# Kernel tuning notes

Measured on AMD Instinct MI355X. Metric: run time of the kernel, lower is better.

Reference implementation:

```python
import jax, jax.numpy as jnp
import numpy as np

D = 2048        # d_model
H = 16          # n_heads
HKV = 4         # n_kv_heads
DH = 128        # d_head = D // H
FF = int(D * 8 / 3)  # 5461, SwiGLU hidden
EPS = 1e-6
ROPE_BASE = 10000.0
B, L = 2, 2048


def rmsnorm(x, w):
    rms = jnp.sqrt(jnp.mean(x * x, axis=-1, keepdims=True) + EPS)
    return x / rms * w


def rope_cos_sin(seq_len):
    inv_freq = 1.0 / (ROPE_BASE ** (jnp.arange(0, DH, 2, dtype=jnp.float32) / DH))
    t = jnp.arange(seq_len, dtype=jnp.float32)
    freqs = t[:, None] * inv_freq[None, :]              # (L, DH/2)
    emb = jnp.concatenate([freqs, freqs], axis=-1)      # (L, DH)
    return jnp.cos(emb), jnp.sin(emb)


def rotate_half(x):
    x1, x2 = jnp.split(x, 2, axis=-1)
    return jnp.concatenate([-x2, x1], axis=-1)


def setup_inputs() -> dict:
    key = jax.random.key(0)
    ks = jax.random.split(key, 10)
    s = 0.02
    return {
        "x": jax.random.normal(ks[0], (B, L, D), dtype=jnp.float32),
        "w_norm1": jnp.ones((D,), dtype=jnp.float32),
        "wq": jax.random.normal(ks[1], (D, H * DH), dtype=jnp.float32) * s,
        "wk": jax.random.normal(ks[2], (D, HKV * DH), dtype=jnp.float32) * s,
        "wv": jax.random.normal(ks[3], (D, HKV * DH), dtype=jnp.float32) * s,
        "wo": jax.random.normal(ks[4], (H * DH, D), dtype=jnp.float32) * s,
        "w_norm2": jnp.ones((D,), dtype=jnp.float32),
        "w_gate": jax.random.normal(ks[5], (D, FF), dtype=jnp.float32) * s,
        "w_up": jax.random.normal(ks[6], (D, FF), dtype=jnp.float32) * s,
        "w_down": jax.random.normal(ks[7], (FF, D), dtype=jnp.float32) * s,
    }


def reference(x, w_norm1, wq, wk, wv, wo, w_norm2, w_gate, w_up, w_down):
    b, l, d = x.shape
    n_rep = H // HKV
    residual = x
    h = rmsnorm(x, w_norm1)
    q = (h @ wq).reshape(b, l, H, DH).transpose(0, 2, 1, 3)    # (B,H,L,DH)
    k = (h @ wk).reshape(b, l, HKV, DH).transpose(0, 2, 1, 3)  # (B,HKV,L,DH)
    v = (h @ wv).reshape(b, l, HKV, DH).transpose(0, 2, 1, 3)
    cos, sin = rope_cos_sin(l)                                 # (L,DH), broadcasts
    q = q * cos + rotate_half(q) * sin
    k = k * cos + rotate_half(k) * sin
    # GQA: repeat KV heads to match Q heads
    k = jnp.repeat(k, n_rep, axis=1)
    v = jnp.repeat(v, n_rep, axis=1)
    scale = 1.0 / np.sqrt(DH)
    attn = jnp.einsum('bhld,bhmd->bhlm', q, k) * scale         # (B,H,L,L)
    causal = jnp.triu(jnp.ones((l, l), dtype=bool), 1)
    attn = jnp.where(causal, -1e9, attn)
    attn = jax.nn.softmax(attn, axis=-1)
    out = jnp.einsum('bhlm,bhmd->bhld', attn, v)
    out = out.transpose(0, 2, 1, 3).reshape(b, l, d)
    x = residual + out @ wo
    residual = x
    h = rmsnorm(x, w_norm2)
    ffn = (jax.nn.silu(h @ w_gate) * (h @ w_up)) @ w_down
    return residual + ffn
```

## Files before the change

kernel.cpp:

```cpp
#include <hip/hip_runtime.h>
#include <stdint.h>

#define BATCH 2
#define SEQ   2048
#define DM    2048
#define NH    16
#define NKV   4
#define DHD   128
#define FFR   5461
#define FFP   5504
#define NTOK  (BATCH*SEQ)
#define QKVW  3072

typedef float f32x4 __attribute__((ext_vector_type(4)));
typedef short bf8v __attribute__((ext_vector_type(8)));
typedef unsigned short us8 __attribute__((ext_vector_type(8)));

__device__ __forceinline__ unsigned short f2bf(float f) {
  unsigned u = __float_as_uint(f);
  u += 0x7fff + ((u >> 16) & 1);
  return (unsigned short)(u >> 16);
}
__device__ __forceinline__ float bf2f(unsigned short b) {
  return __uint_as_float(((unsigned)b) << 16);
}

__device__ __forceinline__ void gload16(const void* g, void* l) {
  __builtin_amdgcn_global_load_lds(
      (const __attribute__((address_space(1))) unsigned int*)(uintptr_t)g,
      (__attribute__((address_space(3))) unsigned int*)(uintptr_t)l,
      16, 0, 0);
}

__global__ __launch_bounds__(256) void k_transpose(const float* __restrict__ S,
    unsigned short* __restrict__ T, int K, int N, int Kpad)
{
  __shared__ float tile[32][33];
  const int n0 = blockIdx.x << 5, k0 = blockIdx.y << 5;
  const int c = threadIdx.x & 31, r0 = threadIdx.x >> 5;
#pragma unroll
  for (int i = 0; i < 4; ++i) {
    int r = r0 + (i << 3);
    float v = 0.f;
    if ((k0 + r) < K && (n0 + c) < N) v = S[(long)(k0 + r) * N + n0 + c];
    tile[r][c] = v;
  }
  __syncthreads();
#pragma unroll
  for (int i = 0; i < 4; ++i) {
    int rr = r0 + (i << 3);
    T[(long)(n0 + rr) * Kpad + k0 + c] = f2bf(tile[c][rr]);
  }
}

__global__ __launch_bounds__(256) void k_transpose_fu(const float* __restrict__ S,
    unsigned short* __restrict__ T, int K, int N, int Kpad, int m01)
{
  __shared__ float tile[32][33];
  const int n0 = blockIdx.x << 5, k0 = blockIdx.y << 5;
  const int c = threadIdx.x & 31, r0 = threadIdx.x >> 5;
#pragma unroll
  for (int i = 0; i < 4; ++i) {
    int r = r0 + (i << 3);
    float v = 0.f;
    if ((k0 + r) < K && (n0 + c) < N) v = S[(long)(k0 + r) * N + n0 + c];
    tile[r][c] = v;
  }
  __syncthreads();
#pragma unroll
  for (int i = 0; i < 4; ++i) {
    int rr = r0 + (i << 3);
    int n = n0 + rr;
    long rp = (long)(n >> 6)*128 + ((n & 63) >> 4)*32 + m01*16 + (n & 15);
    T[rp * Kpad + k0 + c] = f2bf(tile[c][rr]);
  }
}

__global__ __launch_bounds__(256) void k_transpose_v(const unsigned short* __restrict__ KV,
    unsigned short* __restrict__ VT)
{
  __shared__ unsigned short tile[32][36];
  const int kv0 = blockIdx.x << 5, d0 = blockIdx.y << 5;
  const int bz = blockIdx.z;
  const int b = bz >> 2, hkv = bz & 3;
  const int flat = threadIdx.x * 4;
  const int r = flat >> 5, c = flat & 31;
  ushort4 v = *(const ushort4*)(KV + ((long)(b*SEQ + kv0 + r))*QKVW + 2560 + hkv*128 + d0 + c);
  tile[r][c] = v.x; tile[r][c+1] = v.y; tile[r][c+2] = v.z; tile[r][c+3] = v.w;
  __syncthreads();
  ushort4 o;
  o.x = tile[c][r]; o.y = tile[c+1][r]; o.z = tile[c+2][r]; o.w = tile[c+3][r];
  *(ushort4*)(VT + ((long)(bz*128 + d0 + r))*SEQ + kv0 + c) = o;
}

__global__ __launch_bounds__(256) void k_rmsnorm(const float* __restrict__ X,
    const float* __restrict__ W, unsigned short* __restrict__ H)
{
  __shared__ float red[4];
  const long row = blockIdx.x;
  const float* xr = X + row * DM;
  const int tid = threadIdx.x;
  float4 a0 = ((const float4*)xr)[2*tid];
  float4 a1 = ((const float4*)xr)[2*tid+1];
  float ss = a0.x*a0.x + a0.y*a0.y + a0.z*a0.z + a0.w*a0.w
           + a1.x*a1.x + a1.y*a1.y + a1.z*a1.z + a1.w*a1.w;
#pragma unroll
  for (int m = 32; m >= 1; m >>= 1) ss += __shfl_xor(ss, m, 64);
  if ((tid & 63) == 0) red[tid >> 6] = ss;
  __syncthreads();
  float sc = rsqrtf((red[0]+red[1]+red[2]+red[3]) * (1.0f/DM) + 1e-6f);
  float4 w0 = ((const float4*)W)[2*tid];
  float4 w1 = ((const float4*)W)[2*tid+1];
  us8 o;
  o[0]=f2bf(a0.x*sc*w0.x); o[1]=f2bf(a0.y*sc*w0.y); o[2]=f2bf(a0.z*sc*w0.z); o[3]=f2bf(a0.w*sc*w0.w);
  o[4]=f2bf(a1.x*sc*w1.x); o[5]=f2bf(a1.y*sc*w1.y); o[6]=f2bf(a1.z*sc*w1.z); o[7]=f2bf(a1.w*sc*w1.w);
  *(us8*)(H + row*DM + tid*8) = o;
}

__global__ void k_rope_table(float* __restrict__ C, float* __restrict__ S)
{
  int i = blockIdx.x * 256 + threadIdx.x;
  int pos = i >> 6, d = i & 63;
  double inv = exp(-(double)d * (9.210340371976184 / 64.0));
  double ang = (double)pos * inv;
  C[i] = (float)cos(ang);
  S[i] = (float)sin(ang);
}

__global__ __launch_bounds__(256) void k_rope_apply(unsigned short* __restrict__ Q,
    const float* __restrict__ C, const float* __restrict__ S, int nh, int stride, int head0)
{
  long i = (long)blockIdx.x * 256 + threadIdx.x;
  int d = (int)(i & 63);
  long t = i >> 6;
  int hh = (int)(t % nh);
  long bl = t / nh;
  int pos = (int)(bl & (SEQ-1));
  long base = bl * stride + head0 + hh*DHD;
  float c = C[pos*64 + d], s = S[pos*64 + d];
  float x1 = bf2f(Q[base + d]);
  float x2 = bf2f(Q[base + 64 + d]);
  Q[base + d]      = f2bf(x1*c - x2*s);
  Q[base + 64 + d] = f2bf(x2*c + x1*s);
}

template<int EPI>
__global__ __launch_bounds__(256) void k_gemm(const unsigned short* __restrict__ A,
    const unsigned short* __restrict__ BT, void* Cout, const float* __restrict__ Res,
    int K, int ldc)
{
  __shared__ __align__(16) unsigned short As[2][128*64];
  __shared__ __align__(16) unsigned short Bs[2][128*64];
  const int tid = threadIdx.x;
  const int l = tid & 63, w = tid >> 6;
  const int wr = w >> 1, wc = w & 1;
  const int nM = gridDim.x, nN = gridDim.y;
  const int nwg = nM * nN;
  const int bid = blockIdx.y * gridDim.x + blockIdx.x;
  const int q8 = nwg >> 3, r8 = nwg & 7, xcd = bid & 7, off8 = bid >> 3;
  const int wg = (xcd < r8 ? xcd*(q8+1) : r8*(q8+1) + (xcd - r8)*q8) + off8;
  const int colTiles = nM * 4;
  const int fullCols = nN >> 2, rem = nN & 3;
  int sc, inCol, wN;
  if (wg < fullCols * colTiles) { sc = wg / colTiles; inCol = wg % colTiles; wN = 4; }
  else { sc = fullCols; inCol = wg - fullCols * colTiles; wN = rem; }
  const int perSuper = 2 * wN;
  const int sm = inCol / perSuper, t8 = inCol % perSuper;
  const long m0 = (long)(sm*2 + t8 / wN) * 128;
  const long n0 = (long)(sc*4 + t8 % wN) * 128;
  const char* Ab = (const char*)(A + m0 * (long)K);
  const char* Bb = (const char*)(BT + n0 * (long)K);
  f32x4 acc[4][4] = {};
  const long ldab = (long)K * 2;
  const int nk = K >> 6;
  const int srow = w*32 + (l >> 3);
  const int scol = ((l & 7) ^ (srow & 7)) * 16;
  auto STAGE = [&](int buf, int kt) {
    const long kb = (long)kt * 128;
#pragma unroll
    for (int i = 0; i < 4; ++i) {
      gload16(Ab + (long)(srow + i*8)*ldab + kb + scol, &As[buf][(w*32 + i*8)*64]);
      gload16(Bb + (long)(srow + i*8)*ldab + kb + scol, &Bs[buf][(w*32 + i*8)*64]);
    }
  };
  STAGE(0, 0);
  __syncthreads();
  int cur = 0;
  for (int kt = 0; kt < nk; ++kt) {
    if (kt + 1 < nk) STAGE(cur ^ 1, kt + 1);
#pragma unroll
    for (int kk = 0; kk < 2; ++kk) {
      bf8v af[4], bfv[4];
#pragma unroll
      for (int m = 0; m < 4; ++m) {
        int r = wr*64 + m*16 + (l & 15);
        int offb = (kk*64 + (l >> 4)*16) ^ ((r & 7) << 4);
        af[m] = *(const bf8v*)((const char*)&As[cur][0] + r*128 + offb);
      }
#pragma unroll
      for (int n = 0; n < 4; ++n) {
        int cI = wc*64 + n*16 + (l & 15);
        int offb = (kk*64 + (l >> 4)*16) ^ ((cI & 7) << 4);
        bfv[n] = *(const bf8v*)((const char*)&Bs[cur][0] + cI*128 + offb);
      }
#pragma unroll
      for (int m = 0; m < 4; ++m)
#pragma unroll
        for (int n = 0; n < 4; ++n)
          acc[m][n] = __builtin_amdgcn_mfma_f32_16x16x32_bf16(af[m], bfv[n], acc[m][n], 0, 0, 0);
    }
    __syncthreads();
    cur ^= 1;
  }
  if (EPI == 3) {
#pragma unroll
    for (int m = 0; m < 4; ++m)
#pragma unroll
      for (int n = 0; n < 4; n += 2)
#pragma unroll
        for (int r = 0; r < 4; ++r) {
          long row = m0 + wr*64 + m*16 + (l >> 4)*4 + r;
          long col = (n0 >> 1) + (wc*2 + (n >> 1))*16 + (l & 15);
          float g = acc[m][n][r], u = acc[m][n+1][r];
          float sv = g / (1.f + __expf(-g));
          ((unsigned short*)Cout)[row * (long)ldc + col] = f2bf(sv * u);
        }
    return;
  }
#pragma unroll
  for (int m = 0; m < 4; ++m)
#pragma unroll
    for (int n = 0; n < 4; ++n)
#pragma unroll
      for (int r = 0; r < 4; ++r) {
        long row = m0 + wr*64 + m*16 + (l >> 4)*4 + r;
        long col = n0 + wc*64 + n*16 + (l & 15);
        long idx = row * (long)ldc + col;
        if (EPI == 0) ((unsigned short*)Cout)[idx] = f2bf(acc[m][n][r]);
        else          ((float*)Cout)[idx] = Res[idx] + acc[m][n][r];
      }
}

__global__ __launch_bounds__(512) void k_attn(const unsigned short* __restrict__ QKV,
    const unsigned short* __restrict__ VbT, unsigned short* __restrict__ O)
{
  __shared__ __align__(16) unsigned short Ks[2][64*128];
  __shared__ __align__(16) unsigned short Vs[2][128*64];
  __shared__ __align__(16) unsigned short Pl[8][16][64];
  const int tid = threadIdx.x, l = tid & 63, w = tid >> 6;
  const int b = blockIdx.z, h = blockIdx.y;
  const int hkv = h >> 2;
  const float scale = 0.08838834764831845f;
  const unsigned short* Kbase = QKV + (long)b*SEQ*QKVW + 2048 + hkv*128;
  const unsigned short* Vtb = VbT + ((long)(b*NKV + hkv))*128*SEQ;

  for (int half = 0; half < 2; ++half) {
    const int qt = half ? (15 - (int)blockIdx.x) : (int)blockIdx.x;
    const int q0 = qt << 7;
    bf8v qa[4];
    {
      const unsigned short* qp = QKV + ((long)(b*SEQ + q0 + w*16 + (l & 15)))*QKVW + h*DHD + (l >> 4)*8;
#pragma unroll
      for (int kk = 0; kk < 4; ++kk) qa[kk] = *(const bf8v*)(qp + kk*32);
    }
    float m_[4], s_[4];
    f32x4 o_[8] = {};
#pragma unroll
    for (int r = 0; r < 4; ++r) { m_[r] = -1e30f; s_[r] = 0.f; }
    const int T = 2*qt + 2;
    const int qmaxw = q0 + w*16 + 15;

    auto STAGE = [&](int buf, int t) {
      const int kv0 = t << 6;
#pragma unroll
      for (int i = 0; i < 2; ++i) {
        int r = w*8 + i*4 + (l >> 4);
        int blk = (l & 15) ^ (r & 7);
        gload16(Kbase + ((long)(kv0 + r))*QKVW + blk*8, &Ks[buf][(w*8 + i*4)*128]);
      }
#pragma unroll
      for (int i = 0; i < 2; ++i) {
        int r = w*16 + i*8 + (l >> 3);
        int blk = (l & 7) ^ (r & 7);
        gload16(Vtb + (long)r*SEQ + kv0 + blk*8, &Vs[buf][(w*16 + i*8)*64]);
      }
    };
    STAGE(0, 0);
    __syncthreads();
    int cur = 0;
    for (int t = 0; t < T; ++t) {
      const int kv0 = t << 6;
      if (t + 1 < T) STAGE(cur ^ 1, t + 1);
      if (kv0 <= qmaxw) {
        f32x4 sc4[4] = {};
        __builtin_amdgcn_s_setprio(1);
#pragma unroll
        for (int n = 0; n < 4; ++n) {
          int row = n*16 + (l & 15);
          const char* kr = (const char*)&Ks[cur][0] + row*256;
#pragma unroll
          for (int kk = 0; kk < 4; ++kk) {
            int off = (kk*64 + (l >> 4)*16) ^ ((row & 7) << 4);
            bf8v kf = *(const bf8v*)(kr + off);
            sc4[n] = __builtin_amdgcn_mfma_f32_16x16x32_bf16(qa[kk], kf, sc4[n], 0, 0, 0);
          }
        }
        __builtin_amdgcn_s_setprio(0);
        float p[4][4];
        float rmax[4] = {-3e30f, -3e30f, -3e30f, -3e30f};
#pragma unroll
        for (int n = 0; n < 4; ++n) {
          int kv = kv0 + n*16 + (l & 15);
#pragma unroll
          for (int r = 0; r < 4; ++r) {
            int qr = q0 + w*16 + (l >> 4)*4 + r;
            float v = sc4[n][r] * scale;
            if (kv > qr) v = -1e30f;
            p[n][r] = v;
            rmax[r] = fmaxf(rmax[r], v);
          }
        }
#pragma unroll
        for (int r = 0; r < 4; ++r) {
          rmax[r] = fmaxf(rmax[r], __shfl_xor(rmax[r], 1, 64));
          rmax[r] = fmaxf(rmax[r], __shfl_xor(rmax[r], 2, 64));
          rmax[r] = fmaxf(rmax[r], __shfl_xor(rmax[r], 4, 64));
          rmax[r] = fmaxf(rmax[r], __shfl_xor(rmax[r], 8, 64));
        }
        float alpha[4], ps[4];
#pragma unroll
        for (int r = 0; r < 4; ++r) {
          float mn = fmaxf(m_[r], rmax[r]);
          alpha[r] = __expf(m_[r] - mn);
          m_[r] = mn;
          ps[r] = 0.f;
        }
#pragma unroll
        for (int n = 0; n < 4; ++n)
#pragma unroll
          for (int r = 0; r < 4; ++r) {
            float e = __expf(p[n][r] - m_[r]);
            p[n][r] = e;
            ps[r] += e;
          }
#pragma unroll
        for (int r = 0; r < 4; ++r) {
          ps[r] += __shfl_xor(ps[r], 1, 64);
          ps[r] += __shfl_xor(ps[r], 2, 64);
          ps[r] += __shfl_xor(ps[r], 4, 64);
          ps[r] += __shfl_xor(ps[r], 8, 64);
          s_[r] = s_[r]*alpha[r] + ps[r];
        }
#pragma unroll
        for (int g = 0; g < 8; ++g) {
          o_[g][0] *= alpha[0]; o_[g][1] *= alpha[1];
          o_[g][2] *= alpha[2]; o_[g][3] *= alpha[3];
        }
#pragma unroll
        for (int n = 0; n < 4; ++n)
#pragma unroll
          for (int r = 0; r < 4; ++r)
            Pl[w][(l >> 4)*4 + r][n*16 + (l & 15)] = f2bf(p[n][r]);
        __builtin_amdgcn_s_setprio(1);
#pragma unroll
        for (int kk2 = 0; kk2 < 2; ++kk2) {
          bf8v pa = *(const bf8v*)&Pl[w][l & 15][kk2*32 + (l >> 4)*8];
#pragma unroll
          for (int g = 0; g < 8; ++g) {
            int d = g*16 + (l & 15);
            int off = (kk2*64 + (l >> 4)*16) ^ ((d & 7) << 4);
            bf8v vf = *(const bf8v*)((const char*)&Vs[cur][0] + d*128 + off);
            o_[g] = __builtin_amdgcn_mfma_f32_16x16x32_bf16(pa, vf, o_[g], 0, 0, 0);
          }
        }
        __builtin_amdgcn_s_setprio(0);
      }
      __syncthreads();
      cur ^= 1;
    }
#pragma unroll
    for (int g = 0; g < 8; ++g)
#pragma unroll
      for (int r = 0; r < 4; ++r) {
        long row = (long)b*SEQ + q0 + w*16 + (l >> 4)*4 + r;
        O[row*DM + h*DHD + g*16 + (l & 15)] = f2bf(o_[g][r] / s_[r]);
      }
  }
}

extern "C" void kernel_launch(void* const* d_in, const int* in_sizes, int n_in,
                              void* d_out, int out_size, void* d_ws, size_t ws_size,
                              hipStream_t stream)
{
  const float* x   = (const float*)d_in[0];
  const float* wn1 = (const float*)d_in[1];
  const float* wq  = (const float*)d_in[2];
  const float* wk  = (const float*)d_in[3];
  const float* wv  = (const float*)d_in[4];
  const float* wo  = (const float*)d_in[5];
  const float* wn2 = (const float*)d_in[6];
  const float* wg  = (const float*)d_in[7];
  const float* wu  = (const float*)d_in[8];
  const float* wd  = (const float*)d_in[9];
  float* out = (float*)d_out;

  char* p = (char*)d_ws;
  auto alloc = [&](size_t bytes) { char* r = p; p += (bytes + 255) & ~(size_t)255; return r; };
  unsigned short* wqkvT = (unsigned short*)alloc((size_t)QKVW*2048*2);
  unsigned short* woT   = (unsigned short*)alloc((size_t)2048*2048*2);
  unsigned short* wguT  = (unsigned short*)alloc((size_t)2*FFP*2048*2);
  unsigned short* wdT   = (unsigned short*)alloc((size_t)2048*FFP*2);
  unsigned short* hb    = (unsigned short*)alloc((size_t)NTOK*2048*2);
  unsigned short* pr    = (unsigned short*)alloc((size_t)NTOK*FFP*2);
  unsigned short* qkv   = (unsigned short*)alloc((size_t)NTOK*QKVW*2);
  unsigned short* vbT   = (unsigned short*)alloc((size_t)BATCH*NKV*128*SEQ*2);
  unsigned short* ao    = (unsigned short*)alloc((size_t)NTOK*2048*2);
  float* ctab = (float*)alloc((size_t)SEQ*64*4);
  float* stab = (float*)alloc((size_t)SEQ*64*4);

  dim3 blk(256);
  k_transpose<<<dim3(2048/32, 2048/32), blk, 0, stream>>>(wq, wqkvT, 2048, 2048, 2048);
  k_transpose<<<dim3(512/32,  2048/32), blk, 0, stream>>>(wk, wqkvT + (size_t)2048*2048, 2048, 512, 2048);
  k_transpose<<<dim3(512/32,  2048/32), blk, 0, stream>>>(wv, wqkvT + (size_t)2560*2048, 2048, 512, 2048);
  k_transpose<<<dim3(2048/32, 2048/32), blk, 0, stream>>>(wo, woT, 2048, 2048, 2048);
  k_transpose_fu<<<dim3(FFP/32, 2048/32), blk, 0, stream>>>(wg, wguT, 2048, FFR, 2048, 0);
  k_transpose_fu<<<dim3(FFP/32, 2048/32), blk, 0, stream>>>(wu, wguT, 2048, FFR, 2048, 1);
  k_transpose<<<dim3(2048/32, FFP/32),  blk, 0, stream>>>(wd, wdT, FFR, 2048, FFP);

  k_rope_table<<<dim3(SEQ*64/256), blk, 0, stream>>>(ctab, stab);
  k_rmsnorm<<<dim3(NTOK), blk, 0, stream>>>(x, wn1, hb);

  k_gemm<0><<<dim3(32, QKVW/128), blk, 0, stream>>>(hb, wqkvT, qkv, nullptr, 2048, QKVW);

  k_rope_apply<<<dim3(NTOK*NH*64/256),  blk, 0, stream>>>(qkv, ctab, stab, NH, QKVW, 0);
  k_rope_apply<<<dim3(NTOK*NKV*64/256), blk, 0, stream>>>(qkv, ctab, stab, NKV, QKVW, 2048);

  k_transpose_v<<<dim3(SEQ/32, 128/32, BATCH*NKV), blk, 0, stream>>>(qkv, vbT);

  k_attn<<<dim3(8, NH, BATCH), dim3(512), 0, stream>>>(qkv, vbT, ao);

  k_gemm<1><<<dim3(32, 16), blk, 0, stream>>>(ao, woT, (void*)out, x, 2048, 2048);
  k_rmsnorm<<<dim3(NTOK), blk, 0, stream>>>(out, wn2, hb);
  k_gemm<3><<<dim3(32, 2*FFP/128), blk, 0, stream>>>(hb, wguT, pr, nullptr, 2048, FFP);
  k_gemm<1><<<dim3(32, 16), blk, 0, stream>>>(pr, wdT, (void*)out, out, FFP, 2048);
}
```

Baseline: 642.6 us.

## Shrink attention tile to 64 queries, drop double buffering, add lazy rescale

The attention kernel now runs 256-thread blocks over 64-query tiles and launches twice as many blocks. It replaces the double-buffered K/V staging with a single buffer and a sync after each load. It also adds a lazy online-softmax rescale that only updates the running max when a row max grows by more than a threshold. This is meant to raise occupancy, cut LDS use and skip the per-tile rescale work, but it loses the overlap between loading and compute.

```diff
diff --git a/kernel.cpp b/kernel.cpp
--- a/kernel.cpp
+++ b/kernel.cpp
@@ -241,25 +241,26 @@
       }
 }
 
-__global__ __launch_bounds__(512) void k_attn(const unsigned short* __restrict__ QKV,
+__global__ __launch_bounds__(256) void k_attn(const unsigned short* __restrict__ QKV,
     const unsigned short* __restrict__ VbT, unsigned short* __restrict__ O)
 {
-  __shared__ __align__(16) unsigned short Ks[2][64*128];
-  __shared__ __align__(16) unsigned short Vs[2][128*64];
-  __shared__ __align__(16) unsigned short Pl[8][16][64];
+  __shared__ __align__(16) unsigned short Ks[64*128];
+  __shared__ __align__(16) unsigned short Vs[128*64];
+  __shared__ __align__(16) unsigned short Pl[4][16][64];
   const int tid = threadIdx.x, l = tid & 63, w = tid >> 6;
   const int b = blockIdx.z, h = blockIdx.y;
   const int hkv = h >> 2;
+  const int la = l & 15, q = l >> 4;
   const float scale = 0.08838834764831845f;
   const unsigned short* Kbase = QKV + (long)b*SEQ*QKVW + 2048 + hkv*128;
   const unsigned short* Vtb = VbT + ((long)(b*NKV + hkv))*128*SEQ;
 
   for (int half = 0; half < 2; ++half) {
-    const int qt = half ? (15 - (int)blockIdx.x) : (int)blockIdx.x;
-    const int q0 = qt << 7;
+    const int qt = half ? (31 - (int)blockIdx.x) : (int)blockIdx.x;
+    const int q0 = qt << 6;
     bf8v qa[4];
     {
-      const unsigned short* qp = QKV + ((long)(b*SEQ + q0 + w*16 + (l & 15)))*QKVW + h*DHD + (l >> 4)*8;
+      const unsigned short* qp = QKV + ((long)(b*SEQ + q0 + w*16 + la))*QKVW + h*DHD + q*8;
 #pragma unroll
       for (int kk = 0; kk < 4; ++kk) qa[kk] = *(const bf8v*)(qp + kk*32);
     }
@@ -267,123 +268,116 @@
     f32x4 o_[8] = {};
 #pragma unroll
     for (int r = 0; r < 4; ++r) { m_[r] = -1e30f; s_[r] = 0.f; }
-    const int T = 2*qt + 2;
-    const int qmaxw = q0 + w*16 + 15;
-
-    auto STAGE = [&](int buf, int t) {
-      const int kv0 = t << 6;
-#pragma unroll
-      for (int i = 0; i < 2; ++i) {
-        int r = w*8 + i*4 + (l >> 4);
-        int blk = (l & 15) ^ (r & 7);
-        gload16(Kbase + ((long)(kv0 + r))*QKVW + blk*8, &Ks[buf][(w*8 + i*4)*128]);
-      }
-#pragma unroll
-      for (int i = 0; i < 2; ++i) {
-        int r = w*16 + i*8 + (l >> 3);
-        int blk = (l & 7) ^ (r & 7);
-        gload16(Vtb + (long)r*SEQ + kv0 + blk*8, &Vs[buf][(w*16 + i*8)*64]);
-      }
-    };
-    STAGE(0, 0);
-    __syncthreads();
-    int cur = 0;
+    const int T = qt + 1;
+
     for (int t = 0; t < T; ++t) {
       const int kv0 = t << 6;
-      if (t + 1 < T) STAGE(cur ^ 1, t + 1);
-      if (kv0 <= qmaxw) {
-        f32x4 sc4[4] = {};
-        __builtin_amdgcn_s_setprio(1);
-#pragma unroll
-        for (int n = 0; n < 4; ++n) {
-          int row = n*16 + (l & 15);
-          const char* kr = (const char*)&Ks[cur][0] + row*256;
-#pragma unroll
-          for (int kk = 0; kk < 4; ++kk) {
-            int off = (kk*64 + (l >> 4)*16) ^ ((row & 7) << 4);
-            bf8v kf = *(const bf8v*)(kr + off);
-            sc4[n] = __builtin_amdgcn_mfma_f32_16x16x32_bf16(qa[kk], kf, sc4[n], 0, 0, 0);
-          }
-        }
-        __builtin_amdgcn_s_setprio(0);
-        float p[4][4];
-        float rmax[4] = {-3e30f, -3e30f, -3e30f, -3e30f};
-#pragma unroll
-        for (int n = 0; n < 4; ++n) {
-          int kv = kv0 + n*16 + (l & 15);
-#pragma unroll
-          for (int r = 0; r < 4; ++r) {
-            int qr = q0 + w*16 + (l >> 4)*4 + r;
-            float v = sc4[n][r] * scale;
-            if (kv > qr) v = -1e30f;
-            p[n][r] = v;
-            rmax[r] = fmaxf(rmax[r], v);
-          }
-        }
+#pragma unroll
+      for (int i = 0; i < 4; ++i) {
+        int r = w*16 + i*4 + (l >> 4);
+        int blk = (l & 15) ^ (r & 7);
+        gload16(Kbase + ((long)(kv0 + r))*QKVW + blk*8, Ks + (w*16 + i*4)*128);
+      }
+#pragma unroll
+      for (int i = 0; i < 4; ++i) {
+        int r = w*32 + i*8 + (l >> 3);
+        int blk = (l & 7) ^ (r & 7);
+        gload16(Vtb + (long)r*SEQ + kv0 + blk*8, Vs + (w*32 + i*8)*64);
+      }
+      __syncthreads();
+
+      f32x4 sc4[4] = {};
+      __builtin_amdgcn_s_setprio(1);
+#pragma unroll
+      for (int n = 0; n < 4; ++n) {
+        int row = n*16 + la;
+        const char* kr = (const char*)Ks + row*256;
+#pragma unroll
+        for (int kk = 0; kk < 4; ++kk) {
+          int off = (kk*64 + q*16) ^ ((row & 7) << 4);
+          bf8v kf = *(const bf8v*)(kr + off);
+          sc4[n] = __builtin_amdgcn_mfma_f32_16x16x32_bf16(qa[kk], kf, sc4[n], 0, 0, 0);
+        }
+      }
+      __builtin_amdgcn_s_setprio(0);
+      float p[4][4];
+      float rmax[4] = {-3e30f, -3e30f, -3e30f, -3e30f};
+#pragma unroll
+      for (int n = 0; n < 4; ++n) {
+        int kv = kv0 + n*16 + la;
 #pragma unroll
         for (int r = 0; r < 4; ++r) {
-          rmax[r] = fmaxf(rmax[r], __shfl_xor(rmax[r], 1, 64));
-          rmax[r] = fmaxf(rmax[r], __shfl_xor(rmax[r], 2, 64));
-          rmax[r] = fmaxf(rmax[r], __shfl_xor(rmax[r], 4, 64));
-          rmax[r] = fmaxf(rmax[r], __shfl_xor(rmax[r], 8, 64));
-        }
-        float alpha[4], ps[4];
+          int qr = q0 + w*16 + q*4 + r;
+          float v = sc4[n][r] * scale;
+          if (kv > qr) v = -1e30f;
+          p[n][r] = v;
+          rmax[r] = fmaxf(rmax[r], v);
+        }
+      }
+#pragma unroll
+      for (int r = 0; r < 4; ++r) {
+        rmax[r] = fmaxf(rmax[r], __shfl_xor(rmax[r], 1, 64));
+        rmax[r] = fmaxf(rmax[r], __shfl_xor(rmax[r], 2, 64));
+        rmax[r] = fmaxf(rmax[r], __shfl_xor(rmax[r], 4, 64));
+        rmax[r] = fmaxf(rmax[r], __shfl_xor(rmax[r], 8, 64));
+      }
+      bool grow = false;
+#pragma unroll
+      for (int r = 0; r < 4; ++r) grow = grow || (rmax[r] > m_[r] + 8.f);
+      if (__any(grow)) {
 #pragma unroll
         for (int r = 0; r < 4; ++r) {
           float mn = fmaxf(m_[r], rmax[r]);
-          alpha[r] = __expf(m_[r] - mn);
+          float a = __expf(m_[r] - mn);
           m_[r] = mn;
-          ps[r] = 0.f;
-        }
-#pragma unroll
-        for (int n = 0; n < 4; ++n)
-#pragma unroll
-          for (int r = 0; r < 4; ++r) {
-            float e = __expf(p[n][r] - m_[r]);
-            p[n][r] = e;
-            ps[r] += e;
-          }
+          s_[r] *= a;
+          o_[0][r] *= a; o_[1][r] *= a; o_[2][r] *= a; o_[3][r] *= a;
+          o_[4][r] *= a; o_[5][r] *= a; o_[6][r] *= a; o_[7][r] *= a;
+        }
+      }
+      float ps[4] = {0.f, 0.f, 0.f, 0.f};
+#pragma unroll
+      for (int n = 0; n < 4; ++n)
 #pragma unroll
         for (int r = 0; r < 4; ++r) {
-          ps[r] += __shfl_xor(ps[r], 1, 64);
-          ps[r] += __shfl_xor(ps[r], 2, 64);
-          ps[r] += __shfl_xor(ps[r], 4, 64);
-          ps[r] += __shfl_xor(ps[r], 8, 64);
-          s_[r] = s_[r]*alpha[r] + ps[r];
-        }
+          float e = __expf(p[n][r] - m_[r]);
+          p[n][r] = e;
+          ps[r] += e;
+        }
+#pragma unroll
+      for (int r = 0; r < 4; ++r) {
+        ps[r] += __shfl_xor(ps[r], 1, 64);
+        ps[r] += __shfl_xor(ps[r], 2, 64);
+        ps[r] += __shfl_xor(ps[r], 4, 64);
+        ps[r] += __shfl_xor(ps[r], 8, 64);
+        s_[r] += ps[r];
+      }
+#pragma unroll
+      for (int n = 0; n < 4; ++n)
+#pragma unroll
+        for (int r = 0; r < 4; ++r)
+          Pl[w][q*4 + r][n*16 + la] = f2bf(p[n][r]);
+      __builtin_amdgcn_s_setprio(1);
+#pragma unroll
+      for (int kk2 = 0; kk2 < 2; ++kk2) {
+        bf8v pa = *(const bf8v*)&Pl[w][la][kk2*32 + q*8];
 #pragma unroll
         for (int g = 0; g < 8; ++g) {
-          o_[g][0] *= alpha[0]; o_[g][1] *= alpha[1];
-          o_[g][2] *= alpha[2]; o_[g][3] *= alpha[3];
-        }
-#pragma unroll
-        for (int n = 0; n < 4; ++n)
-#pragma unroll
-          for (int r = 0; r < 4; ++r)
-            Pl[w][(l >> 4)*4 + r][n*16 + (l & 15)] = f2bf(p[n][r]);
-        __builtin_amdgcn_s_setprio(1);
-#pragma unroll
-        for (int kk2 = 0; kk2 < 2; ++kk2) {
-          bf8v pa = *(const bf8v*)&Pl[w][l & 15][kk2*32 + (l >> 4)*8];
-#pragma unroll
-          for (int g = 0; g < 8; ++g) {
-            int d = g*16 + (l & 15);
-            int off = (kk2*64 + (l >> 4)*16) ^ ((d & 7) << 4);
-            bf8v vf = *(const bf8v*)((const char*)&Vs[cur][0] + d*128 + off);
-            o_[g] = __builtin_amdgcn_mfma_f32_16x16x32_bf16(pa, vf, o_[g], 0, 0, 0);
-          }
-        }
-        __builtin_amdgcn_s_setprio(0);
-      }
+          int d = g*16 + la;
+          int off = (kk2*64 + q*16) ^ ((d & 7) << 4);
+          bf8v vf = *(const bf8v*)((const char*)Vs + d*128 + off);
+          o_[g] = __builtin_amdgcn_mfma_f32_16x16x32_bf16(pa, vf, o_[g], 0, 0, 0);
+        }
+      }
+      __builtin_amdgcn_s_setprio(0);
       __syncthreads();
-      cur ^= 1;
     }
 #pragma unroll
     for (int g = 0; g < 8; ++g)
 #pragma unroll
       for (int r = 0; r < 4; ++r) {
-        long row = (long)b*SEQ + q0 + w*16 + (l >> 4)*4 + r;
-        O[row*DM + h*DHD + g*16 + (l & 15)] = f2bf(o_[g][r] / s_[r]);
+        long row = (long)b*SEQ + q0 + w*16 + q*4 + r;
+        O[row*DM + h*DHD + g*16 + la] = f2bf(o_[g][r] / s_[r]);
       }
   }
 }
@@ -437,7 +431,7 @@
 
   k_transpose_v<<<dim3(SEQ/32, 128/32, BATCH*NKV), blk, 0, stream>>>(qkv, vbT);
 
-  k_attn<<<dim3(8, NH, BATCH), dim3(512), 0, stream>>>(qkv, vbT, ao);
+  k_attn<<<dim3(16, NH, BATCH), blk, 0, stream>>>(qkv, vbT, ao);
 
   k_gemm<1><<<dim3(32, 16), blk, 0, stream>>>(ao, woT, (void*)out, x, 2048, 2048);
   k_rmsnorm<<<dim3(NTOK), blk, 0, stream>>>(out, wn2, hb);
```

Result: no change. 646.3 us (+0.6%).

## Share K/V tiles across GQA head group in attention and fuse Q RoPE

Applied to the files above, without the earlier changes.

Restructures attention so each block handles one KV head with its four query heads across 64 query rows. Each wave computes two 16-row blocks, so every staged K/V tile is reused by four heads instead of being reloaded per head. RoPE for Q is now applied in-register after loading, which removes the separate Q rope kernel. The online-softmax rescale is skipped unless the row max grows by more than 8, cutting exp and multiply work. The costs are the loss of the causal load-balancing pairing of q-tiles, more registers per wave, and some extra rounding from applying RoPE to bf16 Q.

```diff
diff --git a/kernel.cpp b/kernel.cpp
--- a/kernel.cpp
+++ b/kernel.cpp
@@ -242,150 +242,181 @@
 }
 
 __global__ __launch_bounds__(512) void k_attn(const unsigned short* __restrict__ QKV,
-    const unsigned short* __restrict__ VbT, unsigned short* __restrict__ O)
+    const unsigned short* __restrict__ VbT, unsigned short* __restrict__ O,
+    const float* __restrict__ Ct, const float* __restrict__ St)
 {
   __shared__ __align__(16) unsigned short Ks[2][64*128];
   __shared__ __align__(16) unsigned short Vs[2][128*64];
-  __shared__ __align__(16) unsigned short Pl[8][16][64];
+  __shared__ __align__(16) unsigned short Pl[8][2][16][64];
   const int tid = threadIdx.x, l = tid & 63, w = tid >> 6;
-  const int b = blockIdx.z, h = blockIdx.y;
-  const int hkv = h >> 2;
+  const int b = blockIdx.z, hkv = blockIdx.y;
+  const int h = hkv*4 + (w & 3);
+  const int qh = w >> 2;
+  const int la = l & 15, q = l >> 4;
   const float scale = 0.08838834764831845f;
+  const int qt = blockIdx.x;
+  const int q0 = qt << 6;
   const unsigned short* Kbase = QKV + (long)b*SEQ*QKVW + 2048 + hkv*128;
   const unsigned short* Vtb = VbT + ((long)(b*NKV + hkv))*128*SEQ;
 
-  for (int half = 0; half < 2; ++half) {
-    const int qt = half ? (15 - (int)blockIdx.x) : (int)blockIdx.x;
-    const int q0 = qt << 7;
-    bf8v qa[4];
-    {
-      const unsigned short* qp = QKV + ((long)(b*SEQ + q0 + w*16 + (l & 15)))*QKVW + h*DHD + (l >> 4)*8;
-#pragma unroll
-      for (int kk = 0; kk < 4; ++kk) qa[kk] = *(const bf8v*)(qp + kk*32);
-    }
-    float m_[4], s_[4];
-    f32x4 o_[8] = {};
-#pragma unroll
-    for (int r = 0; r < 4; ++r) { m_[r] = -1e30f; s_[r] = 0.f; }
-    const int T = 2*qt + 2;
-    const int qmaxw = q0 + w*16 + 15;
-
-    auto STAGE = [&](int buf, int t) {
-      const int kv0 = t << 6;
-#pragma unroll
-      for (int i = 0; i < 2; ++i) {
-        int r = w*8 + i*4 + (l >> 4);
-        int blk = (l & 15) ^ (r & 7);
-        gload16(Kbase + ((long)(kv0 + r))*QKVW + blk*8, &Ks[buf][(w*8 + i*4)*128]);
-      }
-#pragma unroll
-      for (int i = 0; i < 2; ++i) {
-        int r = w*16 + i*8 + (l >> 3);
-        int blk = (l & 7) ^ (r & 7);
-        gload16(Vtb + (long)r*SEQ + kv0 + blk*8, &Vs[buf][(w*16 + i*8)*64]);
-      }
-    };
-    STAGE(0, 0);
+  bf8v qa[2][4];
+#pragma unroll
+  for (int rb = 0; rb < 2; ++rb) {
+    const int pos = q0 + qh*32 + rb*16 + la;
+    const unsigned short* qp = QKV + ((long)(b*SEQ + pos))*QKVW + h*DHD + q*8;
+#pragma unroll
+    for (int kk = 0; kk < 4; ++kk) qa[rb][kk] = *(const bf8v*)(qp + kk*32);
+    const float* Cb = Ct + pos*64 + q*8;
+    const float* Sb = St + pos*64 + q*8;
+    float a0[8], a1[8], a2[8], a3[8];
+#pragma unroll
+    for (int j = 0; j < 8; ++j) {
+      a0[j] = bf2f((unsigned short)qa[rb][0][j]);
+      a1[j] = bf2f((unsigned short)qa[rb][1][j]);
+      a2[j] = bf2f((unsigned short)qa[rb][2][j]);
+      a3[j] = bf2f((unsigned short)qa[rb][3][j]);
+    }
+#pragma unroll
+    for (int j = 0; j < 8; ++j) {
+      float c0 = Cb[j], s0 = Sb[j], c1 = Cb[32 + j], s1 = Sb[32 + j];
+      qa[rb][0][j] = (short)f2bf(a0[j]*c0 - a2[j]*s0);
+      qa[rb][1][j] = (short)f2bf(a1[j]*c1 - a3[j]*s1);
+      qa[rb][2][j] = (short)f2bf(a2[j]*c0 + a0[j]*s0);
+      qa[rb][3][j] = (short)f2bf(a3[j]*c1 + a1[j]*s1);
+    }
+  }
+  float m_[2][4], s_[2][4];
+  f32x4 o_[2][8] = {};
+#pragma unroll
+  for (int rb = 0; rb < 2; ++rb)
+#pragma unroll
+    for (int r = 0; r < 4; ++r) { m_[rb][r] = -1e30f; s_[rb][r] = 0.f; }
+  const int T = qt + 1;
+
+  auto STAGE = [&](int buf, int t) {
+    const int kv0 = t << 6;
+#pragma unroll
+    for (int i = 0; i < 2; ++i) {
+      int r = i*32 + w*4 + (l >> 4);
+      int blk = (l & 15) ^ (r & 7);
+      gload16(Kbase + ((long)(kv0 + r))*QKVW + blk*8, &Ks[buf][(i*32 + w*4)*128]);
+    }
+#pragma unroll
+    for (int i = 0; i < 2; ++i) {
+      int r = i*64 + w*8 + (l >> 3);
+      int blk = (l & 7) ^ (r & 7);
+      gload16(Vtb + (long)r*SEQ + kv0 + blk*8, &Vs[buf][(i*64 + w*8)*64]);
+    }
+  };
+  STAGE(0, 0);
+  __syncthreads();
+  int cur = 0;
+
+  for (int t = 0; t < T; ++t) {
+    const int kv0 = t << 6;
+    if (t + 1 < T) STAGE(cur ^ 1, t + 1);
+    f32x4 sc4[2][4] = {};
+    __builtin_amdgcn_s_setprio(1);
+#pragma unroll
+    for (int n = 0; n < 4; ++n) {
+      int row = n*16 + la;
+      const char* kr = (const char*)&Ks[cur][0] + row*256;
+#pragma unroll
+      for (int kk = 0; kk < 4; ++kk) {
+        int off = (kk*64 + q*16) ^ ((row & 7) << 4);
+        bf8v kf = *(const bf8v*)(kr + off);
+        sc4[0][n] = __builtin_amdgcn_mfma_f32_16x16x32_bf16(qa[0][kk], kf, sc4[0][n], 0, 0, 0);
+        sc4[1][n] = __builtin_amdgcn_mfma_f32_16x16x32_bf16(qa[1][kk], kf, sc4[1][n], 0, 0, 0);
+      }
+    }
+    __builtin_amdgcn_s_setprio(0);
+#pragma unroll
+    for (int rb = 0; rb < 2; ++rb) {
+      float p[4][4];
+      float rmax[4] = {-3e30f, -3e30f, -3e30f, -3e30f};
+#pragma unroll
+      for (int n = 0; n < 4; ++n) {
+        int kv = kv0 + n*16 + la;
+#pragma unroll
+        for (int r = 0; r < 4; ++r) {
+          int qr = q0 + qh*32 + rb*16 + q*4 + r;
+          float v = sc4[rb][n][r] * scale;
+          if (kv > qr) v = -1e30f;
+          p[n][r] = v;
+          rmax[r] = fmaxf(rmax[r], v);
+        }
+      }
+#pragma unroll
+      for (int r = 0; r < 4; ++r) {
+        rmax[r] = fmaxf(rmax[r], __shfl_xor(rmax[r], 1, 64));
+        rmax[r] = fmaxf(rmax[r], __shfl_xor(rmax[r], 2, 64));
+        rmax[r] = fmaxf(rmax[r], __shfl_xor(rmax[r], 4, 64));
+        rmax[r] = fmaxf(rmax[r], __shfl_xor(rmax[r], 8, 64));
+      }
+      bool grow = false;
+#pragma unroll
+      for (int r = 0; r < 4; ++r) grow = grow || (rmax[r] > m_[rb][r] + 8.f);
+      if (__any(grow)) {
+#pragma unroll
+        for (int r = 0; r < 4; ++r) {
+          float mn = fmaxf(m_[rb][r], rmax[r]);
+          float a = __expf(m_[rb][r] - mn);
+          m_[rb][r] = mn;
+          s_[rb][r] *= a;
+#pragma unroll
+          for (int g = 0; g < 8; ++g) o_[rb][g][r] *= a;
+        }
+      }
+      float ps[4] = {0.f, 0.f, 0.f, 0.f};
+#pragma unroll
+      for (int n = 0; n < 4; ++n)
+#pragma unroll
+        for (int r = 0; r < 4; ++r) {
+          float e = __expf(p[n][r] - m_[rb][r]);
+          p[n][r] = e;
+          ps[r] += e;
+        }
+#pragma unroll
+      for (int r = 0; r < 4; ++r) {
+        ps[r] += __shfl_xor(ps[r], 1, 64);
+        ps[r] += __shfl_xor(ps[r], 2, 64);
+        ps[r] += __shfl_xor(ps[r], 4, 64);
+        ps[r] += __shfl_xor(ps[r], 8, 64);
+        s_[rb][r] += ps[r];
+      }
+#pragma unroll
+      for (int n = 0; n < 4; ++n)
+#pragma unroll
+        for (int r = 0; r < 4; ++r)
+          Pl[w][rb][q*4 + r][n*16 + la] = f2bf(p[n][r]);
+    }
+    __builtin_amdgcn_s_setprio(1);
+#pragma unroll
+    for (int kk2 = 0; kk2 < 2; ++kk2) {
+      bf8v pa0 = *(const bf8v*)&Pl[w][0][la][kk2*32 + q*8];
+      bf8v pa1 = *(const bf8v*)&Pl[w][1][la][kk2*32 + q*8];
+#pragma unroll
+      for (int g = 0; g < 8; ++g) {
+        int d = g*16 + la;
+        int off = (kk2*64 + q*16) ^ ((d & 7) << 4);
+        bf8v vf = *(const bf8v*)((const char*)&Vs[cur][0] + d*128 + off);
+        o_[0][g] = __builtin_amdgcn_mfma_f32_16x16x32_bf16(pa0, vf, o_[0][g], 0, 0, 0);
+        o_[1][g] = __builtin_amdgcn_mfma_f32_16x16x32_bf16(pa1, vf, o_[1][g], 0, 0, 0);
+      }
+    }
+    __builtin_amdgcn_s_setprio(0);
     __syncthreads();
-    int cur = 0;
-    for (int t = 0; t < T; ++t) {
-      const int kv0 = t << 6;
-      if (t + 1 < T) STAGE(cur ^ 1, t + 1);
-      if (kv0 <= qmaxw) {
-        f32x4 sc4[4] = {};
-        __builtin_amdgcn_s_setprio(1);
-#pragma unroll
-        for (int n = 0; n < 4; ++n) {
-          int row = n*16 + (l & 15);
-          const char* kr = (const char*)&Ks[cur][0] + row*256;
-#pragma unroll
-          for (int kk = 0; kk < 4; ++kk) {
-            int off = (kk*64 + (l >> 4)*16) ^ ((row & 7) << 4);
-            bf8v kf = *(const bf8v*)(kr + off);
-            sc4[n] = __builtin_amdgcn_mfma_f32_16x16x32_bf16(qa[kk], kf, sc4[n], 0, 0, 0);
-          }
-        }
-        __builtin_amdgcn_s_setprio(0);
-        float p[4][4];
-        float rmax[4] = {-3e30f, -3e30f, -3e30f, -3e30f};
-#pragma unroll
-        for (int n = 0; n < 4; ++n) {
-          int kv = kv0 + n*16 + (l & 15);
-#pragma unroll
-          for (int r = 0; r < 4; ++r) {
-            int qr = q0 + w*16 + (l >> 4)*4 + r;
-            float v = sc4[n][r] * scale;
-            if (kv > qr) v = -1e30f;
-            p[n][r] = v;
-            rmax[r] = fmaxf(rmax[r], v);
-          }
-        }
-#pragma unroll
-        for (int r = 0; r < 4; ++r) {
-          rmax[r] = fmaxf(rmax[r], __shfl_xor(rmax[r], 1, 64));
-          rmax[r] = fmaxf(rmax[r], __shfl_xor(rmax[r], 2, 64));
-          rmax[r] = fmaxf(rmax[r], __shfl_xor(rmax[r], 4, 64));
-          rmax[r] = fmaxf(rmax[r], __shfl_xor(rmax[r], 8, 64));
-        }
-        float alpha[4], ps[4];
-#pragma unroll
-        for (int r = 0; r < 4; ++r) {
-          float mn = fmaxf(m_[r], rmax[r]);
-          alpha[r] = __expf(m_[r] - mn);
-          m_[r] = mn;
-          ps[r] = 0.f;
-        }
-#pragma unroll
-        for (int n = 0; n < 4; ++n)
-#pragma unroll
-          for (int r = 0; r < 4; ++r) {
-            float e = __expf(p[n][r] - m_[r]);
-            p[n][r] = e;
-            ps[r] += e;
-          }
-#pragma unroll
-        for (int r = 0; r < 4; ++r) {
-          ps[r] += __shfl_xor(ps[r], 1, 64);
-          ps[r] += __shfl_xor(ps[r], 2, 64);
-          ps[r] += __shfl_xor(ps[r], 4, 64);
-          ps[r] += __shfl_xor(ps[r], 8, 64);
-          s_[r] = s_[r]*alpha[r] + ps[r];
-        }
-#pragma unroll
-        for (int g = 0; g < 8; ++g) {
-          o_[g][0] *= alpha[0]; o_[g][1] *= alpha[1];
-          o_[g][2] *= alpha[2]; o_[g][3] *= alpha[3];
-        }
-#pragma unroll
-        for (int n = 0; n < 4; ++n)
-#pragma unroll
-          for (int r = 0; r < 4; ++r)
-            Pl[w][(l >> 4)*4 + r][n*16 + (l & 15)] = f2bf(p[n][r]);
-        __builtin_amdgcn_s_setprio(1);
-#pragma unroll
-        for (int kk2 = 0; kk2 < 2; ++kk2) {
-          bf8v pa = *(const bf8v*)&Pl[w][l & 15][kk2*32 + (l >> 4)*8];
-#pragma unroll
-          for (int g = 0; g < 8; ++g) {
-            int d = g*16 + (l & 15);
-            int off = (kk2*64 + (l >> 4)*16) ^ ((d & 7) << 4);
-            bf8v vf = *(const bf8v*)((const char*)&Vs[cur][0] + d*128 + off);
-            o_[g] = __builtin_amdgcn_mfma_f32_16x16x32_bf16(pa, vf, o_[g], 0, 0, 0);
-          }
-        }
-        __builtin_amdgcn_s_setprio(0);
-      }
-      __syncthreads();
-      cur ^= 1;
-    }
+    cur ^= 1;
+  }
+#pragma unroll
+  for (int rb = 0; rb < 2; ++rb)
 #pragma unroll
     for (int g = 0; g < 8; ++g)
 #pragma unroll
       for (int r = 0; r < 4; ++r) {
-        long row = (long)b*SEQ + q0 + w*16 + (l >> 4)*4 + r;
-        O[row*DM + h*DHD + g*16 + (l & 15)] = f2bf(o_[g][r] / s_[r]);
-      }
-  }
+        long row = (long)b*SEQ + q0 + qh*32 + rb*16 + q*4 + r;
+        O[row*DM + h*DHD + g*16 + la] = f2bf(o_[rb][g][r] / s_[rb][r]);
+      }
 }
 
 extern "C" void kernel_launch(void* const* d_in, const int* in_sizes, int n_in,
@@ -432,12 +463,11 @@
 
   k_gemm<0><<<dim3(32, QKVW/128), blk, 0, stream>>>(hb, wqkvT, qkv, nullptr, 2048, QKVW);
 
-  k_rope_apply<<<dim3(NTOK*NH*64/256),  blk, 0, stream>>>(qkv, ctab, stab, NH, QKVW, 0);
   k_rope_apply<<<dim3(NTOK*NKV*64/256), blk, 0, stream>>>(qkv, ctab, stab, NKV, QKVW, 2048);
 
   k_transpose_v<<<dim3(SEQ/32, 128/32, BATCH*NKV), blk, 0, stream>>>(qkv, vbT);
 
-  k_attn<<<dim3(8, NH, BATCH), dim3(512), 0, stream>>>(qkv, vbT, ao);
+  k_attn<<<dim3(32, NKV, BATCH), dim3(512), 0, stream>>>(qkv, vbT, ao, ctab, stab);
 
   k_gemm<1><<<dim3(32, 16), blk, 0, stream>>>(ao, woT, (void*)out, x, 2048, 2048);
   k_rmsnorm<<<dim3(NTOK), blk, 0, stream>>>(out, wn2, hb);
```

Result: slower. 671.6 us (+4.5%).
